# Optimization experiments

Hardware: AMD Instinct MI355X
Metric: run time of the kernel (lower is better)

The kernel has to match this reference:

```python
import jax, jax.numpy as jnp
import numpy as np

N_NODES = 50000
N_EDGES = 800000
IN_DIM, FEAT_DIM, HID_DIM, OUT_DIM = 512, 256, 256, 128


def _glorot(key, shape):
    fan_in = shape[-1]
    bound = 1.0 / np.sqrt(fan_in)
    return jax.random.uniform(key, shape, jnp.float32, -bound, bound)


def setup_inputs() -> dict:
    key = jax.random.key(0)
    ks = jax.random.split(key, 12)
    x = jax.random.normal(ks[0], (N_NODES, IN_DIM), jnp.float32)
    edge_index = jax.random.randint(ks[1], (2, N_EDGES), 0, N_NODES, jnp.int64)
    return {
        "x": x,
        "edge_index": edge_index,
        # feature_pre MLP
        "W_pre": _glorot(ks[2], (FEAT_DIM, IN_DIM)),
        "b_pre": jnp.zeros((FEAT_DIM,), jnp.float32),
        "W_pre2": _glorot(ks[3], (HID_DIM, FEAT_DIM)),
        "b_pre2": jnp.zeros((HID_DIM,), jnp.float32),
        # conv_first: SAGEConv(hidden, hidden); lin_l (neighbors, with bias), lin_r (root, no bias)
        "Wl1": _glorot(ks[4], (HID_DIM, HID_DIM)),
        "bl1": jnp.zeros((HID_DIM,), jnp.float32),
        "Wr1": _glorot(ks[5], (HID_DIM, HID_DIM)),
        # conv_out: SAGEConv(hidden, output)
        "Wl2": _glorot(ks[6], (OUT_DIM, HID_DIM)),
        "bl2": jnp.zeros((OUT_DIM,), jnp.float32),
        "Wr2": _glorot(ks[7], (OUT_DIM, HID_DIM)),
    }


def sage_conv(x, src, dst, Wl, bl, Wr):
    # mean-aggregate source features at destination nodes, then linear + root linear
    n = x.shape[0]
    msg = x[src]                                               # [E, D]
    agg = jax.ops.segment_sum(msg, dst, num_segments=n)        # [N, D]
    cnt = jax.ops.segment_sum(jnp.ones((src.shape[0],), x.dtype), dst, num_segments=n)
    mean = agg / jnp.maximum(cnt, 1.0)[:, None]
    return mean @ Wl.T + bl + x @ Wr.T


def reference(x, edge_index, W_pre, b_pre, W_pre2, b_pre2, Wl1, bl1, Wr1, Wl2, bl2, Wr2):
    src, dst = edge_index[0], edge_index[1]
    h = x @ W_pre.T + b_pre
    h = h @ W_pre2.T + b_pre2
    h = jax.nn.relu(sage_conv(h, src, dst, Wl1, bl1, Wr1))
    # dropout is identity in eval mode; layer_num=2 -> no hidden convs
    h = sage_conv(h, src, dst, Wl2, bl2, Wr2)
    # F.normalize(p=2, dim=-1), eps=1e-12
    norm = jnp.maximum(jnp.linalg.norm(h, axis=-1, keepdims=True), 1e-12)
    return h / norm
```

## Files before the change

### kernel.cpp

```cpp
#include <hip/hip_runtime.h>
#include <hip/hip_bf16.h>


typedef __attribute__((ext_vector_type(4))) float f32x4;
typedef __attribute__((ext_vector_type(8))) short s8v;

__device__ __forceinline__ float bf2f(unsigned short u) {
  union { unsigned int i; float f; } v; v.i = ((unsigned int)u) << 16; return v.f;
}
__device__ __forceinline__ unsigned short f2bf(float f) {
  unsigned int u = __builtin_bit_cast(unsigned int, f);
  u += 0x7fffu + ((u >> 16) & 1u);
  return (unsigned short)(u >> 16);
}

__global__ __launch_bounds__(256) void zero_int_kernel(int* __restrict__ p, int n) {
  int i = blockIdx.x * blockDim.x + threadIdx.x;
  const int stride = gridDim.x * blockDim.x;
  for (; i < n; i += stride) p[i] = 0;
}

__global__ __launch_bounds__(256) void count_kernel(const int* __restrict__ dst,
                                                    int* __restrict__ cnt, int E) {
  const int e = blockIdx.x * blockDim.x + threadIdx.x;
  if (e < E) atomicAdd(&cnt[dst[e]], 1);
}

__global__ __launch_bounds__(256) void scan_pass1(const int* __restrict__ cnt,
                                                  int* __restrict__ bsum, int M) {
  __shared__ int red[256];
  const int t = threadIdx.x;
  const int i = blockIdx.x * 256 + t;
  red[t] = (i < M) ? cnt[i] : 0;
  __syncthreads();
  for (int off = 128; off > 0; off >>= 1) {
    if (t < off) red[t] += red[t + off];
    __syncthreads();
  }
  if (t == 0) bsum[blockIdx.x] = red[0];
}

__global__ __launch_bounds__(256) void scan_pass2(const int* __restrict__ bsum,
    int* __restrict__ boff, int* __restrict__ rowptr, int nb, int M, int E) {
  __shared__ int buf[256];
  const int t = threadIdx.x;
  const int v = (t < nb) ? bsum[t] : 0;
  buf[t] = v;
  __syncthreads();
  for (int off = 1; off < 256; off <<= 1) {
    const int add = (t >= off) ? buf[t - off] : 0;
    __syncthreads();
    buf[t] += add;
    __syncthreads();
  }
  if (t < nb) boff[t] = buf[t] - v;
  if (t == 0) rowptr[M] = E;
}

__global__ __launch_bounds__(256) void scan_pass3(int* __restrict__ cnt,
    const int* __restrict__ boff, int* __restrict__ rowptr, int M) {
  __shared__ int buf[256];
  const int t = threadIdx.x;
  const int i = blockIdx.x * 256 + t;
  const int v = (i < M) ? cnt[i] : 0;
  buf[t] = v;
  __syncthreads();
  for (int off = 1; off < 256; off <<= 1) {
    const int add = (t >= off) ? buf[t - off] : 0;
    __syncthreads();
    buf[t] += add;
    __syncthreads();
  }
  if (i < M) {
    rowptr[i] = buf[t] - v + boff[blockIdx.x];
    cnt[i] = 0;
  }
}

__global__ __launch_bounds__(256) void fill_kernel(const int* __restrict__ src,
    const int* __restrict__ dst, const int* __restrict__ rowptr,
    int* __restrict__ cursor, unsigned short* __restrict__ eidx, int E) {
  const int e = blockIdx.x * blockDim.x + threadIdx.x;
  if (e >= E) return;
  const int d = dst[e];
  const int pos = rowptr[d] + atomicAdd(&cursor[d], 1);
  eidx[pos] = (unsigned short)src[e];
}

__global__ __launch_bounds__(256) void combine_w_kernel(const float* __restrict__ Wp,
    const float* __restrict__ Wp2, unsigned short* __restrict__ Wc) {
  __shared__ float wrow[256];
  const int o = blockIdx.x, t = threadIdx.x;
  wrow[t] = Wp2[o * 256 + t];
  __syncthreads();
  float a0 = 0.f, a1 = 0.f;
  for (int m = 0; m < 256; ++m) {
    const float w = wrow[m];
    a0 = fmaf(w, Wp[m * 512 + t], a0);
    a1 = fmaf(w, Wp[m * 512 + 256 + t], a1);
  }
  Wc[o * 512 + t] = f2bf(a0);
  Wc[o * 512 + 256 + t] = f2bf(a1);
}

__global__ __launch_bounds__(256) void combine_b_kernel(const float* __restrict__ Wp2,
    const float* __restrict__ bp, const float* __restrict__ bp2, float* __restrict__ bc) {
  const int o = threadIdx.x;
  float s = 0.f;
  for (int m = 0; m < 256; ++m) s = fmaf(Wp2[o * 256 + m], bp[m], s);
  bc[o] = s + bp2[o];
}

__global__ __launch_bounds__(256) void pack_b1_kernel(const float* __restrict__ Wl1,
    const float* __restrict__ Wr1, unsigned short* __restrict__ Bc1) {
  const int idx = blockIdx.x * 256 + threadIdx.x;
  const int o = idx >> 9, k = idx & 511;
  const float v = (k < 256) ? Wl1[o * 256 + k] : Wr1[o * 256 + (k - 256)];
  Bc1[idx] = f2bf(v);
}

__global__ __launch_bounds__(256) void pack_b2_kernel(const float* __restrict__ Wl2,
    const float* __restrict__ Wr2, unsigned short* __restrict__ Bc2) {
  const int idx = blockIdx.x * 256 + threadIdx.x;
  const int r = idx >> 8, k = idx & 255;
  const float v = (r < 128) ? Wl2[r * 256 + k] : Wr2[(r - 128) * 256 + k];
  Bc2[idx] = f2bf(v);
}

template <int K, int ASTRIDE, int CSTRIDE, int CBASE, bool BIAS_EN, bool RELU_EN, bool A_FP32>
__global__ __launch_bounds__(256) void mfma_gemm(const void* __restrict__ Ap,
    const unsigned short* __restrict__ Bp, const float* __restrict__ bias,
    unsigned short* __restrict__ Cp, int M) {
  __shared__ __align__(16) char smem[4096 + 16384];
  char* const Asb = smem;
  char* const Bsb = smem + 4096;

  const int t = threadIdx.x, w = t >> 6, l = t & 63;
  const int bm = blockIdx.x * 64;
  const int lr = l >> 2;
  const int ls = l & 3;
  const int lss = ls ^ ((l >> 3) & 3);
  const int arow = min(bm + w * 16 + lr, M - 1);
  const int lane15 = l & 15, half = l >> 4;

  float bias_l[4];
  if (BIAS_EN) {
#pragma unroll
    for (int ns = 0; ns < 4; ++ns) bias_l[ns] = bias[w * 64 + ns * 16 + lane15];
  }

  f32x4 acc[4][4];
#pragma unroll
  for (int i = 0; i < 4; ++i)
#pragma unroll
    for (int j = 0; j < 4; ++j) acc[i][j] = f32x4{0.f, 0.f, 0.f, 0.f};

#pragma unroll 1
  for (int k0 = 0; k0 < K; k0 += 32) {
    __syncthreads();
    if (A_FP32) {
      const float* ap = (const float*)Ap + (size_t)arow * ASTRIDE + k0 + lss * 8;
      const float4 f0 = *(const float4*)ap;
      const float4 f1 = *(const float4*)(ap + 4);
      s8v pk;
      pk[0] = (short)f2bf(f0.x); pk[1] = (short)f2bf(f0.y);
      pk[2] = (short)f2bf(f0.z); pk[3] = (short)f2bf(f0.w);
      pk[4] = (short)f2bf(f1.x); pk[5] = (short)f2bf(f1.y);
      pk[6] = (short)f2bf(f1.z); pk[7] = (short)f2bf(f1.w);
      *(s8v*)(Asb + w * 1024 + l * 16) = pk;
    } else {
      const unsigned short* ap =
          (const unsigned short*)Ap + (size_t)arow * ASTRIDE + k0 + lss * 8;
      __builtin_amdgcn_global_load_lds(ap, Asb + w * 1024, 16, 0, 0);
    }
#pragma unroll
    for (int i = 0; i < 4; ++i) {
      const int c = w * 4 + i;
      const unsigned short* bp = Bp + (size_t)(c * 16 + lr) * K + k0 + lss * 8;
      __builtin_amdgcn_global_load_lds(bp, Bsb + c * 1024, 16, 0, 0);
    }
    __syncthreads();

    s8v af[4], bf[4];
#pragma unroll
    for (int ms = 0; ms < 4; ++ms) {
      const int r = ms * 16 + lane15;
      af[ms] = *(const s8v*)(Asb + r * 64 + ((half ^ ((r >> 1) & 3)) << 4));
    }
#pragma unroll
    for (int ns = 0; ns < 4; ++ns) {
      const int r = w * 64 + ns * 16 + lane15;
      bf[ns] = *(const s8v*)(Bsb + r * 64 + ((half ^ ((r >> 1) & 3)) << 4));
    }
#pragma unroll
    for (int ms = 0; ms < 4; ++ms)
#pragma unroll
      for (int ns = 0; ns < 4; ++ns)
        acc[ms][ns] =
            __builtin_amdgcn_mfma_f32_16x16x32_bf16(af[ms], bf[ns], acc[ms][ns], 0, 0, 0);
  }

#pragma unroll
  for (int ms = 0; ms < 4; ++ms)
#pragma unroll
    for (int ns = 0; ns < 4; ++ns) {
      const int col = w * 64 + ns * 16 + lane15;
      f32x4 v = acc[ms][ns];
      if (BIAS_EN) {
#pragma unroll
        for (int r = 0; r < 4; ++r) v[r] += bias_l[ns];
      }
      if (RELU_EN) {
#pragma unroll
        for (int r = 0; r < 4; ++r) v[r] = fmaxf(v[r], 0.f);
      }
#pragma unroll
      for (int r = 0; r < 4; ++r) {
        const int row = bm + ms * 16 + half * 4 + r;
        if (row < M) Cp[(size_t)row * CSTRIDE + CBASE + col] = f2bf(v[r]);
      }
    }
}

__global__ __launch_bounds__(256) void gather_mean256_kernel(
    unsigned short* __restrict__ Acat, const int* __restrict__ rowptr,
    const unsigned short* __restrict__ eidx, int M) {
  const int node = blockIdx.x * 4 + (threadIdx.x >> 6);
  if (node >= M) return;
  const int lane = threadIdx.x & 63;
  const int c4 = lane * 4;
  const int beg = rowptr[node], end = rowptr[node + 1];
  float a0 = 0.f, a1 = 0.f, a2 = 0.f, a3 = 0.f;
  int j = beg;
  for (; j + 1 < end; j += 2) {
    const size_t s0 = eidx[j], s1 = eidx[j + 1];
    const ushort4 v0 = *(const ushort4*)(Acat + s0 * 512 + 256 + c4);
    const ushort4 v1 = *(const ushort4*)(Acat + s1 * 512 + 256 + c4);
    a0 += bf2f(v0.x) + bf2f(v1.x); a1 += bf2f(v0.y) + bf2f(v1.y);
    a2 += bf2f(v0.z) + bf2f(v1.z); a3 += bf2f(v0.w) + bf2f(v1.w);
  }
  if (j < end) {
    const size_t s0 = eidx[j];
    const ushort4 v0 = *(const ushort4*)(Acat + s0 * 512 + 256 + c4);
    a0 += bf2f(v0.x); a1 += bf2f(v0.y); a2 += bf2f(v0.z); a3 += bf2f(v0.w);
  }
  const float inv = 1.0f / fmaxf((float)(end - beg), 1.0f);
  ushort4 o;
  o.x = f2bf(a0 * inv); o.y = f2bf(a1 * inv);
  o.z = f2bf(a2 * inv); o.w = f2bf(a3 * inv);
  *(ushort4*)(Acat + (size_t)node * 512 + c4) = o;
}

__global__ __launch_bounds__(256) void gather_finalize_kernel(
    const unsigned short* __restrict__ Acat, const int* __restrict__ rowptr,
    const unsigned short* __restrict__ eidx, const float* __restrict__ bl2,
    float* __restrict__ out, int M) {
  const int node = blockIdx.x * 4 + (threadIdx.x >> 6);
  if (node >= M) return;
  const int lane = threadIdx.x & 63;
  const int c2 = lane * 2;
  const int beg = rowptr[node], end = rowptr[node + 1];
  float ax = 0.f, ay = 0.f;
  int j = beg;
  for (; j + 1 < end; j += 2) {
    const size_t s0 = eidx[j], s1 = eidx[j + 1];
    const ushort2 v0 = *(const ushort2*)(Acat + s0 * 512 + 256 + c2);
    const ushort2 v1 = *(const ushort2*)(Acat + s1 * 512 + 256 + c2);
    ax += bf2f(v0.x) + bf2f(v1.x); ay += bf2f(v0.y) + bf2f(v1.y);
  }
  if (j < end) {
    const size_t s0 = eidx[j];
    const ushort2 v0 = *(const ushort2*)(Acat + s0 * 512 + 256 + c2);
    ax += bf2f(v0.x); ay += bf2f(v0.y);
  }
  const float inv = 1.0f / fmaxf((float)(end - beg), 1.0f);
  const ushort2 rr = *(const ushort2*)(Acat + (size_t)node * 512 + 384 + c2);
  const float2 b = *(const float2*)&bl2[c2];
  const float vx = fmaf(ax, inv, b.x) + bf2f(rr.x);
  const float vy = fmaf(ay, inv, b.y) + bf2f(rr.y);
  float ss = vx * vx + vy * vy;
#pragma unroll
  for (int off = 32; off > 0; off >>= 1) ss += __shfl_xor(ss, off);
  const float rn = 1.0f / fmaxf(sqrtf(ss), 1e-12f);
  *(float2*)&out[(size_t)node * 128 + c2] = make_float2(vx * rn, vy * rn);
}

extern "C" void kernel_launch(void* const* d_in, const int* in_sizes, int n_in,
                              void* d_out, int out_size, void* d_ws, size_t ws_size,
                              hipStream_t stream) {
  const float* x      = (const float*)d_in[0];
  const int*   ei     = (const int*)d_in[1];
  const float* W_pre  = (const float*)d_in[2];
  const float* b_pre  = (const float*)d_in[3];
  const float* W_pre2 = (const float*)d_in[4];
  const float* b_pre2 = (const float*)d_in[5];
  const float* Wl1    = (const float*)d_in[6];
  const float* bl1    = (const float*)d_in[7];
  const float* Wr1    = (const float*)d_in[8];
  const float* Wl2    = (const float*)d_in[9];
  const float* bl2    = (const float*)d_in[10];
  const float* Wr2    = (const float*)d_in[11];
  float* out = (float*)d_out;

  const int M = in_sizes[0] / 512;
  const int E = in_sizes[1] / 2;
  const int* src = ei;
  const int* dst = ei + E;

  char* p = (char*)d_ws;
  unsigned short* Acat = (unsigned short*)p; p += (size_t)M * 512 * 2;
  unsigned short* H3   = (unsigned short*)p; p += (size_t)M * 256 * 2;
  unsigned short* Wc   = (unsigned short*)p; p += 256 * 512 * 2;
  unsigned short* Bc1  = (unsigned short*)p; p += 256 * 512 * 2;
  unsigned short* Bc2  = (unsigned short*)p; p += 256 * 256 * 2;
  float* bc   = (float*)p; p += 256 * 4;
  int* rowptr = (int*)p;   p += (size_t)(M + 1) * 4;
  int* cnt    = (int*)p;   p += (size_t)M * 4;
  int* bsum   = (int*)p;   p += 256 * 4;
  int* boff   = (int*)p;   p += 256 * 4;
  unsigned short* eidx = (unsigned short*)p;

  const int eblk = (E + 255) / 256;
  const int nb   = (M + 255) / 256;
  const int gx   = (M + 63) / 64;
  const int nblk = (M + 3) / 4;

  zero_int_kernel<<<256, 256, 0, stream>>>(cnt, M);
  count_kernel<<<eblk, 256, 0, stream>>>(dst, cnt, E);
  scan_pass1<<<nb, 256, 0, stream>>>(cnt, bsum, M);
  scan_pass2<<<1, 256, 0, stream>>>(bsum, boff, rowptr, nb, M, E);
  scan_pass3<<<nb, 256, 0, stream>>>(cnt, boff, rowptr, M);
  fill_kernel<<<eblk, 256, 0, stream>>>(src, dst, rowptr, cnt, eidx, E);

  combine_w_kernel<<<256, 256, 0, stream>>>(W_pre, W_pre2, Wc);
  combine_b_kernel<<<1, 256, 0, stream>>>(W_pre2, b_pre, b_pre2, bc);
  pack_b1_kernel<<<512, 256, 0, stream>>>(Wl1, Wr1, Bc1);
  pack_b2_kernel<<<256, 256, 0, stream>>>(Wl2, Wr2, Bc2);

  mfma_gemm<512, 512, 512, 256, true, false, true>
      <<<gx, 256, 0, stream>>>(x, Wc, bc, Acat, M);
  gather_mean256_kernel<<<nblk, 256, 0, stream>>>(Acat, rowptr, eidx, M);
  mfma_gemm<512, 512, 256, 0, true, true, false>
      <<<gx, 256, 0, stream>>>(Acat, Bc1, bl1, H3, M);
  mfma_gemm<256, 256, 512, 256, false, false, false>
      <<<gx, 256, 0, stream>>>(H3, Bc2, nullptr, Acat, M);
  gather_finalize_kernel<<<nblk, 256, 0, stream>>>(Acat, rowptr, eidx, bl2, out, M);
}
```

Measured before the change: 333.3 us.

## Double-buffer GEMM with 64-wide K tiles, fuse weight prep, unroll gathers

The MFMA GEMM moves from single-buffered 32-wide K steps to double-buffered 64-wide K tiles, so the next tile's global-to-LDS loads overlap the current tile's MFMAs and each tile needs one barrier instead of two. The fp32 A path holds its next tile in registers and converts it after compute. The four weight-prep kernels become one launch, and both gather kernels unroll to four neighbors per step for more memory-level parallelism. LDS use grows to about 80KB per block, which may lower occupancy.

```diff
diff --git a/kernel.cpp b/kernel.cpp
--- a/kernel.cpp
+++ b/kernel.cpp
@@ -4,6 +4,10 @@
 
 typedef __attribute__((ext_vector_type(4))) float f32x4;
 typedef __attribute__((ext_vector_type(8))) short s8v;
+
+#define A_BUF_SZ 8192
+#define B_BUF_SZ 32768
+#define B_BASE   (2 * A_BUF_SZ)
 
 __device__ __forceinline__ float bf2f(unsigned short u) {
   union { unsigned int i; float f; } v; v.i = ((unsigned int)u) << 16; return v.f;
@@ -87,61 +91,53 @@
   eidx[pos] = (unsigned short)src[e];
 }
 
-__global__ __launch_bounds__(256) void combine_w_kernel(const float* __restrict__ Wp,
-    const float* __restrict__ Wp2, unsigned short* __restrict__ Wc) {
-  __shared__ float wrow[256];
-  const int o = blockIdx.x, t = threadIdx.x;
-  wrow[t] = Wp2[o * 256 + t];
-  __syncthreads();
-  float a0 = 0.f, a1 = 0.f;
-  for (int m = 0; m < 256; ++m) {
-    const float w = wrow[m];
-    a0 = fmaf(w, Wp[m * 512 + t], a0);
-    a1 = fmaf(w, Wp[m * 512 + 256 + t], a1);
-  }
-  Wc[o * 512 + t] = f2bf(a0);
-  Wc[o * 512 + 256 + t] = f2bf(a1);
-}
-
-__global__ __launch_bounds__(256) void combine_b_kernel(const float* __restrict__ Wp2,
-    const float* __restrict__ bp, const float* __restrict__ bp2, float* __restrict__ bc) {
-  const int o = threadIdx.x;
-  float s = 0.f;
-  for (int m = 0; m < 256; ++m) s = fmaf(Wp2[o * 256 + m], bp[m], s);
-  bc[o] = s + bp2[o];
-}
-
-__global__ __launch_bounds__(256) void pack_b1_kernel(const float* __restrict__ Wl1,
-    const float* __restrict__ Wr1, unsigned short* __restrict__ Bc1) {
-  const int idx = blockIdx.x * 256 + threadIdx.x;
-  const int o = idx >> 9, k = idx & 511;
-  const float v = (k < 256) ? Wl1[o * 256 + k] : Wr1[o * 256 + (k - 256)];
-  Bc1[idx] = f2bf(v);
-}
-
-__global__ __launch_bounds__(256) void pack_b2_kernel(const float* __restrict__ Wl2,
-    const float* __restrict__ Wr2, unsigned short* __restrict__ Bc2) {
-  const int idx = blockIdx.x * 256 + threadIdx.x;
-  const int r = idx >> 8, k = idx & 255;
-  const float v = (r < 128) ? Wl2[r * 256 + k] : Wr2[(r - 128) * 256 + k];
-  Bc2[idx] = f2bf(v);
+__global__ __launch_bounds__(256) void prep_kernel(const float* __restrict__ Wp,
+    const float* __restrict__ Wp2, const float* __restrict__ bp,
+    const float* __restrict__ bp2, const float* __restrict__ Wl1,
+    const float* __restrict__ Wr1, const float* __restrict__ Wl2,
+    const float* __restrict__ Wr2, unsigned short* __restrict__ Wc,
+    float* __restrict__ bc, unsigned short* __restrict__ Bc1,
+    unsigned short* __restrict__ Bc2) {
+  const int b = blockIdx.x, t = threadIdx.x;
+  if (b < 256) {
+    __shared__ float wrow[256];
+    wrow[t] = Wp2[b * 256 + t];
+    __syncthreads();
+    float a0 = 0.f, a1 = 0.f;
+    for (int m = 0; m < 256; ++m) {
+      const float w = wrow[m];
+      a0 = fmaf(w, Wp[m * 512 + t], a0);
+      a1 = fmaf(w, Wp[m * 512 + 256 + t], a1);
+    }
+    Wc[b * 512 + t] = f2bf(a0);
+    Wc[b * 512 + 256 + t] = f2bf(a1);
+  } else if (b == 256) {
+    float s = 0.f;
+    for (int m = 0; m < 256; ++m) s = fmaf(Wp2[t * 256 + m], bp[m], s);
+    bc[t] = s + bp2[t];
+  } else if (b < 769) {
+    const int idx = (b - 257) * 256 + t;
+    const int o = idx >> 9, k = idx & 511;
+    const float v = (k < 256) ? Wl1[o * 256 + k] : Wr1[o * 256 + (k - 256)];
+    Bc1[idx] = f2bf(v);
+  } else {
+    const int idx = (b - 769) * 256 + t;
+    const int r = idx >> 8, k = idx & 255;
+    const float v = (r < 128) ? Wl2[r * 256 + k] : Wr2[(r - 128) * 256 + k];
+    Bc2[idx] = f2bf(v);
+  }
 }
 
 template <int K, int ASTRIDE, int CSTRIDE, int CBASE, bool BIAS_EN, bool RELU_EN, bool A_FP32>
 __global__ __launch_bounds__(256) void mfma_gemm(const void* __restrict__ Ap,
     const unsigned short* __restrict__ Bp, const float* __restrict__ bias,
     unsigned short* __restrict__ Cp, int M) {
-  __shared__ __align__(16) char smem[4096 + 16384];
-  char* const Asb = smem;
-  char* const Bsb = smem + 4096;
+  constexpr int NT = K / 64;
+  __shared__ __align__(16) char smem[2 * A_BUF_SZ + 2 * B_BUF_SZ];
 
   const int t = threadIdx.x, w = t >> 6, l = t & 63;
   const int bm = blockIdx.x * 64;
-  const int lr = l >> 2;
-  const int ls = l & 3;
-  const int lss = ls ^ ((l >> 3) & 3);
-  const int arow = min(bm + w * 16 + lr, M - 1);
-  const int lane15 = l & 15, half = l >> 4;
+  const int lane15 = l & 15, half = (l >> 4) & 3;
 
   float bias_l[4];
   if (BIAS_EN) {
@@ -155,49 +151,102 @@
 #pragma unroll
     for (int j = 0; j < 4; ++j) acc[i][j] = f32x4{0.f, 0.f, 0.f, 0.f};
 
+  auto stageB = [&](char* dstB, int k0) {
+#pragma unroll
+    for (int i = 0; i < 8; ++i) {
+      const int c = i * 256 + t;
+      const int rB = c >> 3;
+      const int sl = (c & 7) ^ (rB & 7);
+      __builtin_amdgcn_global_load_lds(
+          (const unsigned int*)(Bp + (size_t)rB * K + k0 + sl * 8),
+          (unsigned int*)(dstB + i * 4096 + w * 1024), 16, 0, 0);
+    }
+  };
+  auto stageA_bf16 = [&](char* dstA, int k0) {
+#pragma unroll
+    for (int i = 0; i < 2; ++i) {
+      const int c = w * 128 + i * 64 + l;
+      const int rA = c >> 3;
+      const int sl = (c & 7) ^ (rA & 7);
+      const unsigned short* ap = (const unsigned short*)Ap +
+          (size_t)min(bm + rA, M - 1) * ASTRIDE + k0 + sl * 8;
+      __builtin_amdgcn_global_load_lds((const unsigned int*)ap,
+          (unsigned int*)(dstA + w * 2048 + i * 1024), 16, 0, 0);
+    }
+  };
+  const int rAf = t >> 2;
+  const int arowf = min(bm + rAf, M - 1);
+  const int phys0 = ((t & 3) * 2) ^ (rAf & 7);
+  auto loadA_f32 = [&](int k0, float4* ar) {
+    const float* ap = (const float*)Ap + (size_t)arowf * ASTRIDE + k0 + (t & 3) * 16;
+    ar[0] = *(const float4*)(ap + 0);
+    ar[1] = *(const float4*)(ap + 4);
+    ar[2] = *(const float4*)(ap + 8);
+    ar[3] = *(const float4*)(ap + 12);
+  };
+  auto writeA_f32 = [&](char* dstA, const float4* ar) {
+    s8v p0, p1;
+    p0[0] = (short)f2bf(ar[0].x); p0[1] = (short)f2bf(ar[0].y);
+    p0[2] = (short)f2bf(ar[0].z); p0[3] = (short)f2bf(ar[0].w);
+    p0[4] = (short)f2bf(ar[1].x); p0[5] = (short)f2bf(ar[1].y);
+    p0[6] = (short)f2bf(ar[1].z); p0[7] = (short)f2bf(ar[1].w);
+    p1[0] = (short)f2bf(ar[2].x); p1[1] = (short)f2bf(ar[2].y);
+    p1[2] = (short)f2bf(ar[2].z); p1[3] = (short)f2bf(ar[2].w);
+    p1[4] = (short)f2bf(ar[3].x); p1[5] = (short)f2bf(ar[3].y);
+    p1[6] = (short)f2bf(ar[3].z); p1[7] = (short)f2bf(ar[3].w);
+    *(s8v*)(dstA + (rAf * 8 + phys0) * 16) = p0;
+    *(s8v*)(dstA + (rAf * 8 + (phys0 ^ 1)) * 16) = p1;
+  };
+
+  stageB(smem + B_BASE, 0);
+  if (A_FP32) {
+    float4 ar[4];
+    loadA_f32(0, ar);
+    writeA_f32(smem, ar);
+  } else {
+    stageA_bf16(smem, 0);
+  }
+  __syncthreads();
+
+  int cur = 0;
 #pragma unroll 1
-  for (int k0 = 0; k0 < K; k0 += 32) {
-    __syncthreads();
-    if (A_FP32) {
-      const float* ap = (const float*)Ap + (size_t)arow * ASTRIDE + k0 + lss * 8;
-      const float4 f0 = *(const float4*)ap;
-      const float4 f1 = *(const float4*)(ap + 4);
-      s8v pk;
-      pk[0] = (short)f2bf(f0.x); pk[1] = (short)f2bf(f0.y);
-      pk[2] = (short)f2bf(f0.z); pk[3] = (short)f2bf(f0.w);
-      pk[4] = (short)f2bf(f1.x); pk[5] = (short)f2bf(f1.y);
-      pk[6] = (short)f2bf(f1.z); pk[7] = (short)f2bf(f1.w);
-      *(s8v*)(Asb + w * 1024 + l * 16) = pk;
-    } else {
-      const unsigned short* ap =
-          (const unsigned short*)Ap + (size_t)arow * ASTRIDE + k0 + lss * 8;
-      __builtin_amdgcn_global_load_lds(ap, Asb + w * 1024, 16, 0, 0);
-    }
-#pragma unroll
-    for (int i = 0; i < 4; ++i) {
-      const int c = w * 4 + i;
-      const unsigned short* bp = Bp + (size_t)(c * 16 + lr) * K + k0 + lss * 8;
-      __builtin_amdgcn_global_load_lds(bp, Bsb + c * 1024, 16, 0, 0);
-    }
-    __syncthreads();
-
-    s8v af[4], bf[4];
-#pragma unroll
-    for (int ms = 0; ms < 4; ++ms) {
-      const int r = ms * 16 + lane15;
-      af[ms] = *(const s8v*)(Asb + r * 64 + ((half ^ ((r >> 1) & 3)) << 4));
-    }
-#pragma unroll
-    for (int ns = 0; ns < 4; ++ns) {
-      const int r = w * 64 + ns * 16 + lane15;
-      bf[ns] = *(const s8v*)(Bsb + r * 64 + ((half ^ ((r >> 1) & 3)) << 4));
-    }
-#pragma unroll
-    for (int ms = 0; ms < 4; ++ms)
+  for (int tt = 0; tt < NT; ++tt) {
+    char* const Ac = smem + cur * A_BUF_SZ;
+    char* const Bc = smem + B_BASE + cur * B_BUF_SZ;
+    char* const An = smem + (cur ^ 1) * A_BUF_SZ;
+    char* const Bn = smem + B_BASE + (cur ^ 1) * B_BUF_SZ;
+    const bool more = (tt + 1 < NT);
+
+    float4 ar[4];
+    if (more) {
+      stageB(Bn, (tt + 1) * 64);
+      if (A_FP32) loadA_f32((tt + 1) * 64, ar);
+      else stageA_bf16(An, (tt + 1) * 64);
+    }
+
+#pragma unroll
+    for (int ksub = 0; ksub < 2; ++ksub) {
+      const int spx = (ksub * 4 + half) ^ (lane15 & 7);
+      s8v af[4], bv[4];
+#pragma unroll
+      for (int ms = 0; ms < 4; ++ms)
+        af[ms] = *(const s8v*)(Ac + (ms * 16 + lane15) * 128 + spx * 16);
 #pragma unroll
       for (int ns = 0; ns < 4; ++ns)
-        acc[ms][ns] =
-            __builtin_amdgcn_mfma_f32_16x16x32_bf16(af[ms], bf[ns], acc[ms][ns], 0, 0, 0);
+        bv[ns] = *(const s8v*)(Bc + (w * 64 + ns * 16 + lane15) * 128 + spx * 16);
+#pragma unroll
+      for (int ms = 0; ms < 4; ++ms)
+#pragma unroll
+        for (int ns = 0; ns < 4; ++ns)
+          acc[ms][ns] =
+              __builtin_amdgcn_mfma_f32_16x16x32_bf16(af[ms], bv[ns], acc[ms][ns], 0, 0, 0);
+    }
+
+    if (more) {
+      if (A_FP32) writeA_f32(An, ar);
+      __syncthreads();
+    }
+    cur ^= 1;
   }
 
 #pragma unroll
@@ -232,14 +281,18 @@
   const int beg = rowptr[node], end = rowptr[node + 1];
   float a0 = 0.f, a1 = 0.f, a2 = 0.f, a3 = 0.f;
   int j = beg;
-  for (; j + 1 < end; j += 2) {
-    const size_t s0 = eidx[j], s1 = eidx[j + 1];
+  for (; j + 3 < end; j += 4) {
+    const size_t s0 = eidx[j], s1 = eidx[j + 1], s2 = eidx[j + 2], s3 = eidx[j + 3];
     const ushort4 v0 = *(const ushort4*)(Acat + s0 * 512 + 256 + c4);
     const ushort4 v1 = *(const ushort4*)(Acat + s1 * 512 + 256 + c4);
-    a0 += bf2f(v0.x) + bf2f(v1.x); a1 += bf2f(v0.y) + bf2f(v1.y);
-    a2 += bf2f(v0.z) + bf2f(v1.z); a3 += bf2f(v0.w) + bf2f(v1.w);
-  }
-  if (j < end) {
+    const ushort4 v2 = *(const ushort4*)(Acat + s2 * 512 + 256 + c4);
+    const ushort4 v3 = *(const ushort4*)(Acat + s3 * 512 + 256 + c4);
+    a0 += (bf2f(v0.x) + bf2f(v1.x)) + (bf2f(v2.x) + bf2f(v3.x));
+    a1 += (bf2f(v0.y) + bf2f(v1.y)) + (bf2f(v2.y) + bf2f(v3.y));
+    a2 += (bf2f(v0.z) + bf2f(v1.z)) + (bf2f(v2.z) + bf2f(v3.z));
+    a3 += (bf2f(v0.w) + bf2f(v1.w)) + (bf2f(v2.w) + bf2f(v3.w));
+  }
+  for (; j < end; ++j) {
     const size_t s0 = eidx[j];
     const ushort4 v0 = *(const ushort4*)(Acat + s0 * 512 + 256 + c4);
     a0 += bf2f(v0.x); a1 += bf2f(v0.y); a2 += bf2f(v0.z); a3 += bf2f(v0.w);
@@ -262,13 +315,16 @@
   const int beg = rowptr[node], end = rowptr[node + 1];
   float ax = 0.f, ay = 0.f;
   int j = beg;
-  for (; j + 1 < end; j += 2) {
-    const size_t s0 = eidx[j], s1 = eidx[j + 1];
+  for (; j + 3 < end; j += 4) {
+    const size_t s0 = eidx[j], s1 = eidx[j + 1], s2 = eidx[j + 2], s3 = eidx[j + 3];
     const ushort2 v0 = *(const ushort2*)(Acat + s0 * 512 + 256 + c2);
     const ushort2 v1 = *(const ushort2*)(Acat + s1 * 512 + 256 + c2);
-    ax += bf2f(v0.x) + bf2f(v1.x); ay += bf2f(v0.y) + bf2f(v1.y);
-  }
-  if (j < end) {
+    const ushort2 v2 = *(const ushort2*)(Acat + s2 * 512 + 256 + c2);
+    const ushort2 v3 = *(const ushort2*)(Acat + s3 * 512 + 256 + c2);
+    ax += (bf2f(v0.x) + bf2f(v1.x)) + (bf2f(v2.x) + bf2f(v3.x));
+    ay += (bf2f(v0.y) + bf2f(v1.y)) + (bf2f(v2.y) + bf2f(v3.y));
+  }
+  for (; j < end; ++j) {
     const size_t s0 = eidx[j];
     const ushort2 v0 = *(const ushort2*)(Acat + s0 * 512 + 256 + c2);
     ax += bf2f(v0.x); ay += bf2f(v0.y);
@@ -332,10 +388,8 @@
   scan_pass3<<<nb, 256, 0, stream>>>(cnt, boff, rowptr, M);
   fill_kernel<<<eblk, 256, 0, stream>>>(src, dst, rowptr, cnt, eidx, E);
 
-  combine_w_kernel<<<256, 256, 0, stream>>>(W_pre, W_pre2, Wc);
-  combine_b_kernel<<<1, 256, 0, stream>>>(W_pre2, b_pre, b_pre2, bc);
-  pack_b1_kernel<<<512, 256, 0, stream>>>(Wl1, Wr1, Bc1);
-  pack_b2_kernel<<<256, 256, 0, stream>>>(Wl2, Wr2, Bc2);
+  prep_kernel<<<1025, 256, 0, stream>>>(W_pre, W_pre2, b_pre, b_pre2,
+                                        Wl1, Wr1, Wl2, Wr2, Wc, bc, Bc1, Bc2);
 
   mfma_gemm<512, 512, 512, 256, true, false, true>
       <<<gx, 256, 0, stream>>>(x, Wc, bc, Acat, M);
```

Result: faster. 275.5 us (-17.3%).
